# Kernel tuning notes

Hardware: AMD Instinct MI355X
Metric: run time of the kernel (lower is better)

Reference implementation:

```python
import jax, jax.numpy as jnp
import numpy as np

DIM_NODES = 128
DIM_EDGES = 64

def rms_norm(x, weight):
    eps = jnp.finfo(x.dtype).eps  # torch nn.RMSNorm default eps
    var = jnp.mean(jnp.square(x), axis=-1, keepdims=True)
    return x * jax.lax.rsqrt(var + eps) * weight

def setup_inputs() -> dict:
    key = jax.random.key(0)
    ks = jax.random.split(key, 6)
    B, N = 2, 512
    edges = jax.random.normal(ks[0], (B, N, N, DIM_EDGES), dtype=jnp.float32)
    nodes = jax.random.normal(ks[1], (B, N, DIM_NODES), dtype=jnp.float32)
    g_node = jnp.ones((DIM_NODES,), dtype=jnp.float32)
    g_edge = jnp.ones((DIM_EDGES,), dtype=jnp.float32)
    din = 2 * DIM_NODES + DIM_EDGES
    W = jax.random.normal(ks[2], (din, DIM_EDGES), dtype=jnp.float32) / np.sqrt(din)
    b = jax.random.normal(ks[3], (DIM_EDGES,), dtype=jnp.float32) * 0.01
    return {"edges": edges, "nodes": nodes, "g_node": g_node, "g_edge": g_edge, "W": W, "b": b}

def reference(edges, nodes, g_node, g_edge, W, b):
    # RMSNorms
    nodes_n = rms_norm(nodes, g_node)          # [B, N, dn]
    edges_n = rms_norm(edges, g_edge)          # [B, N, N, de]
    dn = nodes.shape[-1]
    # Decompose Linear over concat([rows, cols, edges]) into three matmuls
    # summed via broadcasting -- same math as cat+Linear, no O(N^2 * 2dn) blowup.
    Wr, Wc, We = W[:dn], W[dn:2 * dn], W[2 * dn:]
    row_proj = jnp.einsum('bid,de->bie', nodes_n, Wr)   # [B, N, de]
    col_proj = jnp.einsum('bjd,de->bje', nodes_n, Wc)   # [B, N, de]
    edge_proj = jnp.einsum('bijd,de->bije', edges_n, We)  # [B, N, N, de]
    out = edge_proj + row_proj[:, :, None, :] + col_proj[:, None, :, :] + b
    return out
```

## Files before the change

### kernel.cpp

```cpp
#include <hip/hip_runtime.h>
#include <hip/hip_bf16.h>

#define DN 128
#define DE 64
#define NN 512

typedef __bf16 bf16x8 __attribute__((ext_vector_type(8)));
typedef float  f32x4  __attribute__((ext_vector_type(4)));

__global__ void prep_kernel(const float* __restrict__ nodes,
                            const float* __restrict__ g_node,
                            const float* __restrict__ g_edge,
                            const float* __restrict__ W,
                            const float* __restrict__ bias,
                            float* __restrict__ rp, float* __restrict__ cp,
                            __bf16* __restrict__ weg) {
    const int l = threadIdx.x;
    if (blockIdx.x == 1024) {
        const int kg = l >> 4;
        for (int kh = 0; kh < 2; ++kh)
            for (int ct = 0; ct < 4; ++ct) {
                const int f = kh * 4 + ct;
                #pragma unroll
                for (int e = 0; e < 8; ++e) {
                    const int k   = kh * 32 + (e >> 2) * 16 + kg * 4 + (e & 3);
                    const int col = ct * 16 + (l & 15);
                    weg[(f * 64 + l) * 8 + e] =
                        (__bf16)(g_edge[k] * W[(2 * DN + k) * DE + col]);
                }
            }
        return;
    }
    const int row = blockIdx.x;
    __shared__ float nn[DN];

    float x0 = nodes[row * DN + l];
    float x1 = nodes[row * DN + l + 64];
    float ssq = x0 * x0 + x1 * x1;
    #pragma unroll
    for (int m = 1; m < 64; m <<= 1) ssq += __shfl_xor(ssq, m, 64);
    float scale = rsqrtf(ssq * (1.0f / DN) + 1.1920929e-7f);
    nn[l]      = x0 * scale * g_node[l];
    nn[l + 64] = x1 * scale * g_node[l + 64];
    __syncthreads();

    float accr = bias[l];
    float accc = 0.0f;
    #pragma unroll 4
    for (int d = 0; d < DN; ++d) {
        float nd = nn[d];
        accr += nd * W[d * DE + l];
        accc += nd * W[(DN + d) * DE + l];
    }
    rp[row * DE + l] = accr;
    cp[row * DE + l] = accc;
}

__global__ __launch_bounds__(256) void main_kernel(
    const float* __restrict__ edges, const float* __restrict__ rp,
    const float* __restrict__ cp, const __bf16* __restrict__ weg,
    float* __restrict__ out) {
    __shared__ float lds[4096];
    const int bid = blockIdx.x;
    const int row = bid >> 3;
    const int t   = threadIdx.x;
    const int w   = t >> 6;
    const int l   = t & 63;
    const int r16 = l & 15;
    const int kg  = l >> 4;
    const int jt0 = (bid & 7) * 64;
    const int bN  = (row >> 9) << 9;

    const float* tile = edges + ((size_t)row * NN + jt0) * DE;

    #pragma unroll
    for (int i = 0; i < 4; ++i) {
        const int C = w * 256 + i * 64 + l;
        const int r = C >> 4;
        const int q = (C & 15) ^ (r & 15);
        __builtin_amdgcn_global_load_lds(
            (const __attribute__((address_space(1))) void*)(tile + r * DE + q * 4),
            (__attribute__((address_space(3))) void*)(&lds[(w * 256 + i * 64) * 4]),
            16, 0, 0);
    }

    bf16x8 wf[8];
    #pragma unroll
    for (int f = 0; f < 8; ++f)
        wf[f] = *reinterpret_cast<const bf16x8*>(weg + (f * 64 + l) * 8);

    const int j = jt0 + w * 16 + r16;
    const float* cprow = cp + (size_t)(bN + j) * DE + kg * 4;
    f32x4 cpv[4];
    #pragma unroll
    for (int c = 0; c < 4; ++c)
        cpv[c] = *reinterpret_cast<const f32x4*>(cprow + c * 16);

    f32x4 rpv[4];
    #pragma unroll
    for (int c = 0; c < 4; ++c)
        rpv[c] = *reinterpret_cast<const f32x4*>(rp + row * DE + c * 16 + kg * 4);

    asm volatile("s_waitcnt vmcnt(0)" ::: "memory");

    const int R = w * 16 + r16;
    f32x4 x[4];
    #pragma unroll
    for (int m = 0; m < 4; ++m) {
        const int q = (m * 4 + kg) ^ r16;
        x[m] = *reinterpret_cast<const f32x4*>(&lds[R * 64 + q * 4]);
    }

    float ssq = 0.0f;
    #pragma unroll
    for (int m = 0; m < 4; ++m)
        #pragma unroll
        for (int e = 0; e < 4; ++e) ssq += x[m][e] * x[m][e];
    ssq += __shfl_xor(ssq, 16, 64);
    ssq += __shfl_xor(ssq, 32, 64);
    const float scale = rsqrtf(ssq * (1.0f / DE) + 1.1920929e-7f);

    bf16x8 a0, a1;
    #pragma unroll
    for (int e = 0; e < 4; ++e) {
        a0[e]     = (__bf16)x[0][e];
        a0[e + 4] = (__bf16)x[1][e];
        a1[e]     = (__bf16)x[2][e];
        a1[e + 4] = (__bf16)x[3][e];
    }

    #pragma unroll
    for (int c = 0; c < 4; ++c) {
        f32x4 z = {0.f, 0.f, 0.f, 0.f};
        z = __builtin_amdgcn_mfma_f32_16x16x32_bf16(wf[c],     a0, z, 0, 0, 0);
        z = __builtin_amdgcn_mfma_f32_16x16x32_bf16(wf[4 + c], a1, z, 0, 0, 0);
        f32x4 o;
        #pragma unroll
        for (int r = 0; r < 4; ++r)
            o[r] = z[r] * scale + rpv[c][r] + cpv[c][r];
        const int qo = (c * 4 + kg) ^ r16;
        *reinterpret_cast<f32x4*>(&lds[R * 64 + qo * 4]) = o;
    }

    asm volatile("s_waitcnt lgkmcnt(0)" ::: "memory");

    float* otile = out + ((size_t)row * NN + jt0) * DE;
    #pragma unroll
    for (int i = 0; i < 4; ++i) {
        const int C = w * 256 + i * 64 + l;
        const int r = C >> 4;
        const int q = (C & 15) ^ (r & 15);
        f32x4 v = *reinterpret_cast<const f32x4*>(&lds[C * 4]);
        *reinterpret_cast<f32x4*>(otile + r * DE + q * 4) = v;
    }
}

extern "C" void kernel_launch(void* const* d_in, const int* in_sizes, int n_in,
                              void* d_out, int out_size, void* d_ws, size_t ws_size,
                              hipStream_t stream) {
    const float* edges  = (const float*)d_in[0];
    const float* nodes  = (const float*)d_in[1];
    const float* g_node = (const float*)d_in[2];
    const float* g_edge = (const float*)d_in[3];
    const float* W      = (const float*)d_in[4];
    const float* bias   = (const float*)d_in[5];
    float* out = (float*)d_out;

    float*  rp  = (float*)d_ws;
    float*  cp  = rp + 1024 * DE;
    __bf16* weg = (__bf16*)(cp + 1024 * DE);

    prep_kernel<<<dim3(1025), dim3(64), 0, stream>>>(nodes, g_node, g_edge, W,
                                                     bias, rp, cp, weg);
    main_kernel<<<dim3(8192), dim3(256), 0, stream>>>(edges, rp, cp, weg, out);
}
```

Before: 61.25 us.

## Double-buffer edge tiles per wave with software-pipelined loads across four iterations

Each wave now processes four 16-row tiles in a loop instead of one. The next tile's global-to-LDS load and the next column-projection loads are issued before the current tile is computed, using two LDS buffers per wave and explicit vmcnt waits. This amortises the weight-fragment and row-projection loads over four tiles and cuts the grid from 8192 to 2048 blocks, aiming to hide load latency inside a block. In exchange the kernel uses twice the LDS per block, carries more registers, and relies on hand-counted vmcnt values and sched barriers, which may reduce occupancy.

New measurement: 105.7 us. +72.6%, slower.

```diff
diff --git a/kernel.cpp b/kernel.cpp
--- a/kernel.cpp
+++ b/kernel.cpp
@@ -56,102 +56,131 @@
     cp[row * DE + l] = accc;
 }
 
-__global__ __launch_bounds__(256) void main_kernel(
+__global__ __launch_bounds__(256, 4) void main_kernel(
     const float* __restrict__ edges, const float* __restrict__ rp,
     const float* __restrict__ cp, const __bf16* __restrict__ weg,
     float* __restrict__ out) {
-    __shared__ float lds[4096];
+    __shared__ float lds[8192];
     const int bid = blockIdx.x;
-    const int row = bid >> 3;
-    const int t   = threadIdx.x;
-    const int w   = t >> 6;
-    const int l   = t & 63;
+    const int row = bid >> 1;
+    const int t4  = threadIdx.x;
+    const int w   = t4 >> 6;
+    const int l   = t4 & 63;
     const int r16 = l & 15;
     const int kg  = l >> 4;
-    const int jt0 = (bid & 7) * 64;
+    const int jb  = (bid & 1) * 256 + w * 64;
     const int bN  = (row >> 9) << 9;
 
-    const float* tile = edges + ((size_t)row * NN + jt0) * DE;
-
-    #pragma unroll
-    for (int i = 0; i < 4; ++i) {
-        const int C = w * 256 + i * 64 + l;
-        const int r = C >> 4;
-        const int q = (C & 15) ^ (r & 15);
-        __builtin_amdgcn_global_load_lds(
-            (const __attribute__((address_space(1))) void*)(tile + r * DE + q * 4),
-            (__attribute__((address_space(3))) void*)(&lds[(w * 256 + i * 64) * 4]),
-            16, 0, 0);
-    }
+    float* wlds = &lds[w * 2048];
+    const float* tbase = edges + ((size_t)row * NN + jb) * DE;
+    float*       obase = out   + ((size_t)row * NN + jb) * DE;
 
     bf16x8 wf[8];
     #pragma unroll
     for (int f = 0; f < 8; ++f)
         wf[f] = *reinterpret_cast<const bf16x8*>(weg + (f * 64 + l) * 8);
 
-    const int j = jt0 + w * 16 + r16;
-    const float* cprow = cp + (size_t)(bN + j) * DE + kg * 4;
-    f32x4 cpv[4];
-    #pragma unroll
-    for (int c = 0; c < 4; ++c)
-        cpv[c] = *reinterpret_cast<const f32x4*>(cprow + c * 16);
-
     f32x4 rpv[4];
     #pragma unroll
     for (int c = 0; c < 4; ++c)
         rpv[c] = *reinterpret_cast<const f32x4*>(rp + row * DE + c * 16 + kg * 4);
 
-    asm volatile("s_waitcnt vmcnt(0)" ::: "memory");
-
-    const int R = w * 16 + r16;
-    f32x4 x[4];
-    #pragma unroll
-    for (int m = 0; m < 4; ++m) {
-        const int q = (m * 4 + kg) ^ r16;
-        x[m] = *reinterpret_cast<const f32x4*>(&lds[R * 64 + q * 4]);
-    }
-
-    float ssq = 0.0f;
-    #pragma unroll
-    for (int m = 0; m < 4; ++m)
-        #pragma unroll
-        for (int e = 0; e < 4; ++e) ssq += x[m][e] * x[m][e];
-    ssq += __shfl_xor(ssq, 16, 64);
-    ssq += __shfl_xor(ssq, 32, 64);
-    const float scale = rsqrtf(ssq * (1.0f / DE) + 1.1920929e-7f);
-
-    bf16x8 a0, a1;
-    #pragma unroll
-    for (int e = 0; e < 4; ++e) {
-        a0[e]     = (__bf16)x[0][e];
-        a0[e + 4] = (__bf16)x[1][e];
-        a1[e]     = (__bf16)x[2][e];
-        a1[e + 4] = (__bf16)x[3][e];
-    }
-
-    #pragma unroll
-    for (int c = 0; c < 4; ++c) {
-        f32x4 z = {0.f, 0.f, 0.f, 0.f};
-        z = __builtin_amdgcn_mfma_f32_16x16x32_bf16(wf[c],     a0, z, 0, 0, 0);
-        z = __builtin_amdgcn_mfma_f32_16x16x32_bf16(wf[4 + c], a1, z, 0, 0, 0);
-        f32x4 o;
-        #pragma unroll
-        for (int r = 0; r < 4; ++r)
-            o[r] = z[r] * scale + rpv[c][r] + cpv[c][r];
-        const int qo = (c * 4 + kg) ^ r16;
-        *reinterpret_cast<f32x4*>(&lds[R * 64 + qo * 4]) = o;
-    }
-
-    asm volatile("s_waitcnt lgkmcnt(0)" ::: "memory");
-
-    float* otile = out + ((size_t)row * NN + jt0) * DE;
+    const float* cpbase = cp + (size_t)(bN + jb + r16) * DE + kg * 4;
+
     #pragma unroll
     for (int i = 0; i < 4; ++i) {
-        const int C = w * 256 + i * 64 + l;
+        const int C = i * 64 + l;
         const int r = C >> 4;
-        const int q = (C & 15) ^ (r & 15);
-        f32x4 v = *reinterpret_cast<const f32x4*>(&lds[C * 4]);
-        *reinterpret_cast<f32x4*>(otile + r * DE + q * 4) = v;
+        const int q = (C & 15) ^ r;
+        __builtin_amdgcn_global_load_lds(
+            (const __attribute__((address_space(1))) void*)(tbase + r * DE + q * 4),
+            (__attribute__((address_space(3))) void*)(&wlds[i * 256]),
+            16, 0, 0);
+    }
+    f32x4 cpv[2][4];
+    #pragma unroll
+    for (int c = 0; c < 4; ++c)
+        cpv[0][c] = *reinterpret_cast<const f32x4*>(cpbase + c * 16);
+
+    __builtin_amdgcn_sched_barrier(0);
+
+    #pragma unroll
+    for (int t = 0; t < 4; ++t) {
+        const int p = t & 1;
+        if (t < 3) {
+            #pragma unroll
+            for (int i = 0; i < 4; ++i) {
+                const int C = i * 64 + l;
+                const int r = C >> 4;
+                const int q = (C & 15) ^ r;
+                __builtin_amdgcn_global_load_lds(
+                    (const __attribute__((address_space(1))) void*)
+                        (tbase + ((t + 1) * 16 + r) * DE + q * 4),
+                    (__attribute__((address_space(3))) void*)
+                        (&wlds[(p ^ 1) * 1024 + i * 256]),
+                    16, 0, 0);
+            }
+            #pragma unroll
+            for (int c = 0; c < 4; ++c)
+                cpv[p ^ 1][c] = *reinterpret_cast<const f32x4*>(
+                    cpbase + (t + 1) * 16 * DE + c * 16);
+        }
+        __builtin_amdgcn_sched_barrier(0);
+        if (t == 0)      asm volatile("s_waitcnt vmcnt(8)"  ::: "memory");
+        else if (t < 3)  asm volatile("s_waitcnt vmcnt(12)" ::: "memory");
+        else             asm volatile("s_waitcnt vmcnt(4)"  ::: "memory");
+        __builtin_amdgcn_sched_barrier(0);
+
+        f32x4 x[4];
+        #pragma unroll
+        for (int m = 0; m < 4; ++m) {
+            const int q = (m * 4 + kg) ^ r16;
+            x[m] = *reinterpret_cast<const f32x4*>(&wlds[p * 1024 + r16 * 64 + q * 4]);
+        }
+
+        float ssq = 0.0f;
+        #pragma unroll
+        for (int m = 0; m < 4; ++m)
+            #pragma unroll
+            for (int e = 0; e < 4; ++e) ssq += x[m][e] * x[m][e];
+        ssq += __shfl_xor(ssq, 16, 64);
+        ssq += __shfl_xor(ssq, 32, 64);
+        const float scale = rsqrtf(ssq * (1.0f / DE) + 1.1920929e-7f);
+
+        bf16x8 a0, a1;
+        #pragma unroll
+        for (int e = 0; e < 4; ++e) {
+            a0[e]     = (__bf16)x[0][e];
+            a0[e + 4] = (__bf16)x[1][e];
+            a1[e]     = (__bf16)x[2][e];
+            a1[e + 4] = (__bf16)x[3][e];
+        }
+
+        #pragma unroll
+        for (int c = 0; c < 4; ++c) {
+            f32x4 z = {0.f, 0.f, 0.f, 0.f};
+            z = __builtin_amdgcn_mfma_f32_16x16x32_bf16(wf[c],     a0, z, 0, 0, 0);
+            z = __builtin_amdgcn_mfma_f32_16x16x32_bf16(wf[4 + c], a1, z, 0, 0, 0);
+            f32x4 o;
+            #pragma unroll
+            for (int r = 0; r < 4; ++r)
+                o[r] = z[r] * scale + rpv[c][r] + cpv[p][c][r];
+            const int qo = (c * 4 + kg) ^ r16;
+            *reinterpret_cast<f32x4*>(&wlds[p * 1024 + r16 * 64 + qo * 4]) = o;
+        }
+
+        asm volatile("s_waitcnt lgkmcnt(0)" ::: "memory");
+        __builtin_amdgcn_sched_barrier(0);
+
+        #pragma unroll
+        for (int i = 0; i < 4; ++i) {
+            const int C = i * 64 + l;
+            const int r = C >> 4;
+            const int q = (C & 15) ^ r;
+            f32x4 v = *reinterpret_cast<const f32x4*>(&wlds[p * 1024 + C * 4]);
+            *reinterpret_cast<f32x4*>(obase + (t * 16 + r) * DE + q * 4) = v;
+        }
+        __builtin_amdgcn_sched_barrier(0);
     }
 }
 
@@ -172,5 +201,5 @@
 
     prep_kernel<<<dim3(1025), dim3(64), 0, stream>>>(nodes, g_node, g_edge, W,
                                                      bias, rp, cp, weg);
-    main_kernel<<<dim3(8192), dim3(256), 0, stream>>>(edges, rp, cp, weg, out);
+    main_kernel<<<dim3(2048), dim3(256), 0, stream>>>(edges, rp, cp, weg, out);
 }
```
